# Kernel tuning notes

Measured on AMD Instinct MI355X. Metric: run time of the kernel, lower is better.

Reference implementation:

```python
import jax, jax.numpy as jnp
import numpy as np

D_MODEL = 1024
N_HEADS = 16
D_HEAD = D_MODEL // N_HEADS  # 64
SCALE = 1.0 / float(np.sqrt(D_HEAD))


def setup_inputs() -> dict:
    key = jax.random.key(0)
    kx, kq, kk, kv, ko = jax.random.split(key, 5)
    B, L = 1, 4096
    x = jax.random.normal(kx, (B, L, D_MODEL), dtype=jnp.float32)
    init = 0.02  # small init so softmax isn't saturated
    Wq = jax.random.normal(kq, (D_MODEL, D_MODEL), dtype=jnp.float32) * init
    Wk = jax.random.normal(kk, (D_MODEL, D_MODEL), dtype=jnp.float32) * init
    Wv = jax.random.normal(kv, (D_MODEL, D_MODEL), dtype=jnp.float32) * init
    Wo = jax.random.normal(ko, (D_MODEL, D_MODEL), dtype=jnp.float32) * init
    return {"x": x, "Wq": Wq, "Wk": Wk, "Wv": Wv, "Wo": Wo}


def reference(x, Wq, Wk, Wv, Wo):
    # x: [B, L, d_model]; torch Linear (no bias): y = x @ W.T
    B, L, _ = x.shape

    def split_heads(t):  # [B, L, d_model] -> [B, H, L, Dh]
        return t.reshape(B, L, N_HEADS, D_HEAD).transpose(0, 2, 1, 3)

    q = split_heads(x @ Wq.T)
    k = split_heads(x @ Wk.T)
    v = split_heads(x @ Wv.T)

    # Full (non-flash) attention: explicit [B, H, L, L] scores (causal=False, eval dropout=0)
    scores = jnp.einsum("bhld,bhmd->bhlm", q, k) * SCALE
    attn = jax.nn.softmax(scores, axis=-1)
    out = jnp.einsum("bhlm,bhmd->bhld", attn, v)

    out = out.transpose(0, 2, 1, 3).reshape(B, L, D_MODEL)
    return out @ Wo.T
```

## Files before the change

kernel.cpp:

```cpp
#include <hip/hip_runtime.h>

typedef _Float16 f16_t;
typedef _Float16 f16x4 __attribute__((ext_vector_type(4)));
typedef _Float16 f16x8 __attribute__((ext_vector_type(8)));
typedef float f32x4 __attribute__((ext_vector_type(4)));

#define D_MODEL 1024
#define LSEQ 4096
#define NH 16
#define DH 64
#define QSCALE 0.18033688011112042f

#define GLDS16(g, l)                                                     \
    __builtin_amdgcn_global_load_lds(                                    \
        (const __attribute__((address_space(1))) void*)(g),              \
        (__attribute__((address_space(3))) void*)(l), 16, 0, 0)

#define WAIT_VM0() asm volatile("s_waitcnt vmcnt(0)" ::: "memory")

__global__ __launch_bounds__(256) void cvt_x(const float* __restrict__ in,
                                             f16_t* __restrict__ out, int n) {
    int i = (blockIdx.x * 256 + threadIdx.x) * 4;
    if (i + 3 < n) {
        float4 v = *(const float4*)&in[i];
        alignas(8) f16_t o4[4] = {(f16_t)v.x, (f16_t)v.y, (f16_t)v.z, (f16_t)v.w};
        *(uint2*)&out[i] = *(const uint2*)o4;
    }
}

__global__ __launch_bounds__(256) void cvt_w4(const float* __restrict__ w0,
                                              const float* __restrict__ w1,
                                              const float* __restrict__ w2,
                                              const float* __restrict__ w3,
                                              f16_t* __restrict__ out) {
    const int q = blockIdx.y;
    const float* src = (q == 0) ? w0 : (q == 1) ? w1 : (q == 2) ? w2 : w3;
    const float scale = (q == 0) ? QSCALE : 1.f;
    int i = (blockIdx.x * 256 + threadIdx.x) * 4;
    float4 v = *(const float4*)&src[i];
    alignas(8) f16_t o4[4] = {(f16_t)(v.x * scale), (f16_t)(v.y * scale),
                              (f16_t)(v.z * scale), (f16_t)(v.w * scale)};
    *(uint2*)&out[(size_t)q * (D_MODEL * D_MODEL) + i] = *(const uint2*)o4;
}

__global__ __launch_bounds__(256, 2) void gemm_f16(const f16_t* __restrict__ A,
                                                   const f16_t* __restrict__ B,
                                                   void* __restrict__ Cout,
                                                   int M, int N, int K, int mode) {
    __shared__ f16_t As[2][128 * 32];
    __shared__ f16_t Bs[2][128 * 32];

    const int tid  = threadIdx.x;
    const int wave = tid >> 6;
    const int lane = tid & 63;
    const int quad = lane >> 4;
    const int l16  = lane & 15;
    const int wm = (wave & 1) * 64;
    const int wn = (wave >> 1) * 64;
    const int bm = blockIdx.x * 128;
    const int bn = blockIdx.y * 128;

    f32x4 acc[4][4] = {};
    const int nk = K / 32;

    auto stage = [&](int kt, int b) {
        const int c0 = wave * 2;
        GLDS16(&A[(size_t)(bm + c0 * 16 + l16) * K + kt * 32 + quad * 8],
               &As[b][c0 * 512]);
        GLDS16(&A[(size_t)(bm + (c0 + 1) * 16 + l16) * K + kt * 32 + quad * 8],
               &As[b][(c0 + 1) * 512]);
        GLDS16(&B[(size_t)(bn + c0 * 16 + l16) * K + kt * 32 + quad * 8],
               &Bs[b][c0 * 512]);
        GLDS16(&B[(size_t)(bn + (c0 + 1) * 16 + l16) * K + kt * 32 + quad * 8],
               &Bs[b][(c0 + 1) * 512]);
    };

    stage(0, 0);
    for (int kt = 0; kt < nk; ++kt) {
        const int cb = kt & 1;
        WAIT_VM0();
        __syncthreads();
        if (kt + 1 < nk) stage(kt + 1, cb ^ 1);

        f16x8 af[4], bfr[4];
#pragma unroll
        for (int mt = 0; mt < 4; ++mt)
            af[mt] = *(const f16x8*)&As[cb][((wm >> 4) + mt) * 512 + lane * 8];
#pragma unroll
        for (int nt = 0; nt < 4; ++nt)
            bfr[nt] = *(const f16x8*)&Bs[cb][((wn >> 4) + nt) * 512 + lane * 8];
#pragma unroll
        for (int mt = 0; mt < 4; ++mt)
#pragma unroll
            for (int nt = 0; nt < 4; ++nt)
                acc[mt][nt] = __builtin_amdgcn_mfma_f32_16x16x32_f16(
                    af[mt], bfr[nt], acc[mt][nt], 0, 0, 0);
    }

#pragma unroll
    for (int mt = 0; mt < 4; ++mt)
#pragma unroll
        for (int nt = 0; nt < 4; ++nt)
#pragma unroll
            for (int r = 0; r < 4; ++r) {
                int row = bm + wm + mt * 16 + quad * 4 + r;
                int col = bn + wn + nt * 16 + l16;
                float v = acc[mt][nt][r];
                if (mode == 0) {
                    ((f16_t*)Cout)[((size_t)(col >> 6) * M + row) * 64 + (col & 63)] =
                        (f16_t)v;
                } else {
                    ((float*)Cout)[(size_t)row * N + col] = v;
                }
            }
}

__global__ __launch_bounds__(256) void transpose_v(const f16_t* __restrict__ vh,
                                                   f16_t* __restrict__ vt) {
    __shared__ f16_t Ts[64][72];
    const int t = threadIdx.x;
    const int lt = blockIdx.x;
    const int head = blockIdx.y;

#pragma unroll
    for (int i = 0; i < 2; ++i) {
        int idx = t + i * 256;
        int row = idx >> 3, part = idx & 7;
        *(uint4*)&Ts[row][part * 8] =
            *(const uint4*)&vh[((size_t)head * LSEQ + lt * 64 + row) * DH + part * 8];
    }
    __syncthreads();
#pragma unroll
    for (int i = 0; i < 2; ++i) {
        int idx = t + i * 256;
        int d = idx >> 3, part = idx & 7;
        alignas(16) f16_t p8[8];
#pragma unroll
        for (int j = 0; j < 8; ++j) p8[j] = Ts[part * 8 + j][d];
        *(uint4*)&vt[((size_t)head * DH + d) * LSEQ + lt * 64 + part * 8] =
            *(const uint4*)p8;
    }
}

__global__ __launch_bounds__(256, 2) void attn_kernel(const f16_t* __restrict__ qh,
                                                      const f16_t* __restrict__ kh,
                                                      const f16_t* __restrict__ vt,
                                                      f16_t* __restrict__ ao) {
    __shared__ f16_t Ks[2][8 * 512];
    __shared__ f16_t Vs[2][8 * 512];
    __shared__ f16_t Ps[4][32][72];

    const int tid  = threadIdx.x;
    const int wave = tid >> 6;
    const int lane = tid & 63;
    const int quad = lane >> 4;
    const int l16  = lane & 15;

    const int id = blockIdx.x;
    const int head = (id & 7) * 2 + ((id >> 3) & 1);
    const int qrow0 = (id >> 4) * 128 + wave * 32;

    const f16_t* Q  = qh + (size_t)head * LSEQ * DH;
    const f16_t* K  = kh + (size_t)head * LSEQ * DH;
    const f16_t* Vt = vt + (size_t)head * DH * LSEQ;

    f16x8 qf[2][2];
#pragma unroll
    for (int qt = 0; qt < 2; ++qt)
#pragma unroll
        for (int kc = 0; kc < 2; ++kc)
            qf[qt][kc] = *(const f16x8*)
                &Q[(size_t)(qrow0 + qt * 16 + l16) * DH + kc * 32 + quad * 8];

    f32x4 o[4][2] = {};
    float lp[2] = {0.f, 0.f};

    auto stage = [&](int kt, int b) {
        const int j0 = wave * 2;
#pragma unroll
        for (int jj = 0; jj < 2; ++jj) {
            const int j = j0 + jj, mt = j >> 1, kc = j & 1;
            GLDS16(&K[(size_t)(kt * 64 + mt * 16 + l16) * DH + kc * 32 + quad * 8],
                   &Ks[b][j * 512]);
            GLDS16(&Vt[(size_t)(mt * 16 + l16) * LSEQ + kt * 64 + kc * 32 + quad * 8],
                   &Vs[b][j * 512]);
        }
    };

    const int NT = LSEQ / 64;
    stage(0, 0);
    for (int kt = 0; kt < NT; ++kt) {
        const int cb = kt & 1;
        WAIT_VM0();
        __syncthreads();
        if (kt + 1 < NT) stage(kt + 1, cb ^ 1);

        f16x8 kf[4][2], vf[4][2];
#pragma unroll
        for (int mt = 0; mt < 4; ++mt)
#pragma unroll
            for (int kc = 0; kc < 2; ++kc)
                kf[mt][kc] = *(const f16x8*)&Ks[cb][(mt * 2 + kc) * 512 + lane * 8];
#pragma unroll
        for (int dt = 0; dt < 4; ++dt)
#pragma unroll
            for (int kc = 0; kc < 2; ++kc)
                vf[dt][kc] = *(const f16x8*)&Vs[cb][(dt * 2 + kc) * 512 + lane * 8];

        f32x4 s[4][2] = {};
#pragma unroll
        for (int mt = 0; mt < 4; ++mt)
#pragma unroll
            for (int qt = 0; qt < 2; ++qt)
#pragma unroll
                for (int kc = 0; kc < 2; ++kc)
                    s[mt][qt] = __builtin_amdgcn_mfma_f32_16x16x32_f16(
                        kf[mt][kc], qf[qt][kc], s[mt][qt], 0, 0, 0);

#pragma unroll
        for (int mt = 0; mt < 4; ++mt)
#pragma unroll
            for (int qt = 0; qt < 2; ++qt) {
                float e0 = __builtin_amdgcn_exp2f(s[mt][qt][0]);
                float e1 = __builtin_amdgcn_exp2f(s[mt][qt][1]);
                float e2 = __builtin_amdgcn_exp2f(s[mt][qt][2]);
                float e3 = __builtin_amdgcn_exp2f(s[mt][qt][3]);
                lp[qt] += (e0 + e1) + (e2 + e3);
                f16x4 p = {(f16_t)e0, (f16_t)e1, (f16_t)e2, (f16_t)e3};
                *(f16x4*)&Ps[wave][qt * 16 + l16][mt * 16 + quad * 4] = p;
            }
        __builtin_amdgcn_wave_barrier();

        f16x8 pf[2][2];
#pragma unroll
        for (int qt = 0; qt < 2; ++qt)
#pragma unroll
            for (int kc = 0; kc < 2; ++kc)
                pf[qt][kc] = *(const f16x8*)
                    &Ps[wave][qt * 16 + l16][kc * 32 + quad * 8];

#pragma unroll
        for (int dt = 0; dt < 4; ++dt)
#pragma unroll
            for (int qt = 0; qt < 2; ++qt)
#pragma unroll
                for (int kc = 0; kc < 2; ++kc)
                    o[dt][qt] = __builtin_amdgcn_mfma_f32_16x16x32_f16(
                        vf[dt][kc], pf[qt][kc], o[dt][qt], 0, 0, 0);
        __builtin_amdgcn_wave_barrier();
    }

#pragma unroll
    for (int qt = 0; qt < 2; ++qt) {
        float t = lp[qt];
        t += __shfl_xor(t, 16, 64);
        t += __shfl_xor(t, 32, 64);
        lp[qt] = 1.f / t;
    }
#pragma unroll
    for (int dt = 0; dt < 4; ++dt)
#pragma unroll
        for (int qt = 0; qt < 2; ++qt) {
            f16x4 ov = {(f16_t)(o[dt][qt][0] * lp[qt]),
                        (f16_t)(o[dt][qt][1] * lp[qt]),
                        (f16_t)(o[dt][qt][2] * lp[qt]),
                        (f16_t)(o[dt][qt][3] * lp[qt])};
            int qrow = qrow0 + qt * 16 + l16;
            *(f16x4*)&ao[(size_t)qrow * D_MODEL + head * 64 + dt * 16 + quad * 4] = ov;
        }
}

extern "C" void kernel_launch(void* const* d_in, const int* in_sizes, int n_in,
                              void* d_out, int out_size, void* d_ws, size_t ws_size,
                              hipStream_t stream) {
    const float* x  = (const float*)d_in[0];
    const float* Wq = (const float*)d_in[1];
    const float* Wk = (const float*)d_in[2];
    const float* Wv = (const float*)d_in[3];
    const float* Wo = (const float*)d_in[4];

    f16_t* xb = (f16_t*)d_ws;
    f16_t* wq = xb + (size_t)LSEQ * D_MODEL;
    f16_t* wo = wq + (size_t)3 * D_MODEL * D_MODEL;
    f16_t* qh = wo + (size_t)D_MODEL * D_MODEL;
    f16_t* kh = qh + (size_t)LSEQ * D_MODEL;
    f16_t* vh = kh + (size_t)LSEQ * D_MODEL;
    f16_t* vt = vh + (size_t)LSEQ * D_MODEL;
    f16_t* ao = vt + (size_t)LSEQ * D_MODEL;

    const int nx = LSEQ * D_MODEL;
    cvt_x<<<nx / 1024, 256, 0, stream>>>(x, xb, nx);
    cvt_w4<<<dim3(D_MODEL * D_MODEL / 1024, 4), 256, 0, stream>>>(Wq, Wk, Wv, Wo, wq);

    gemm_f16<<<dim3(LSEQ / 128, 3 * D_MODEL / 128), 256, 0, stream>>>(
        xb, wq, qh, LSEQ, 3 * D_MODEL, D_MODEL, 0);

    transpose_v<<<dim3(LSEQ / 64, NH), 256, 0, stream>>>(vh, vt);

    attn_kernel<<<dim3((LSEQ / 128) * NH), 256, 0, stream>>>(qh, kh, vt, ao);

    gemm_f16<<<dim3(LSEQ / 128, D_MODEL / 128), 256, 0, stream>>>(
        ao, wo, d_out, LSEQ, D_MODEL, D_MODEL, 1);
}
```

Baseline: 273.2 us.

## Triple-buffer GEMM and attention loads and double attention query tile per wave

Both the projection GEMM and the attention kernel move from double to triple buffering of their LDS tiles. They wait with a partial vmcnt so one future stage stays in flight while the current tile is consumed. The attention kernel also gives each wave 64 query rows instead of 32, so every K/V tile loaded into LDS is reused over twice as many queries. That halves the grid to 256 blocks at one block per CU, which cuts latency hiding and raises register pressure. The GEMM's launch bound is raised to 3 blocks per CU to match its larger shared-memory footprint.

```diff
diff --git a/kernel.cpp b/kernel.cpp
--- a/kernel.cpp
+++ b/kernel.cpp
@@ -16,7 +16,7 @@
         (const __attribute__((address_space(1))) void*)(g),              \
         (__attribute__((address_space(3))) void*)(l), 16, 0, 0)
 
-#define WAIT_VM0() asm volatile("s_waitcnt vmcnt(0)" ::: "memory")
+#define WAIT_VM(n) asm volatile("s_waitcnt vmcnt(" #n ")" ::: "memory")
 
 __global__ __launch_bounds__(256) void cvt_x(const float* __restrict__ in,
                                              f16_t* __restrict__ out, int n) {
@@ -43,12 +43,12 @@
     *(uint2*)&out[(size_t)q * (D_MODEL * D_MODEL) + i] = *(const uint2*)o4;
 }
 
-__global__ __launch_bounds__(256, 2) void gemm_f16(const f16_t* __restrict__ A,
+__global__ __launch_bounds__(256, 3) void gemm_f16(const f16_t* __restrict__ A,
                                                    const f16_t* __restrict__ B,
                                                    void* __restrict__ Cout,
                                                    int M, int N, int K, int mode) {
-    __shared__ f16_t As[2][128 * 32];
-    __shared__ f16_t Bs[2][128 * 32];
+    __shared__ alignas(16) f16_t As[3][128 * 32];
+    __shared__ alignas(16) f16_t Bs[3][128 * 32];
 
     const int tid  = threadIdx.x;
     const int wave = tid >> 6;
@@ -76,11 +76,13 @@
     };
 
     stage(0, 0);
+    stage(1, 1);
     for (int kt = 0; kt < nk; ++kt) {
-        const int cb = kt & 1;
-        WAIT_VM0();
+        const int cb = kt % 3;
+        if (kt < nk - 1) WAIT_VM(4);
+        else             WAIT_VM(0);
         __syncthreads();
-        if (kt + 1 < nk) stage(kt + 1, cb ^ 1);
+        if (kt + 2 < nk) stage(kt + 2, (kt + 2) % 3);
 
         f16x8 af[4], bfr[4];
 #pragma unroll
@@ -142,13 +144,13 @@
     }
 }
 
-__global__ __launch_bounds__(256, 2) void attn_kernel(const f16_t* __restrict__ qh,
+__global__ __launch_bounds__(256, 1) void attn_kernel(const f16_t* __restrict__ qh,
                                                       const f16_t* __restrict__ kh,
                                                       const f16_t* __restrict__ vt,
                                                       f16_t* __restrict__ ao) {
-    __shared__ f16_t Ks[2][8 * 512];
-    __shared__ f16_t Vs[2][8 * 512];
-    __shared__ f16_t Ps[4][32][72];
+    __shared__ alignas(16) f16_t Ks[3][8 * 512];
+    __shared__ alignas(16) f16_t Vs[3][8 * 512];
+    __shared__ alignas(16) f16_t Ps[4][64][72];
 
     const int tid  = threadIdx.x;
     const int wave = tid >> 6;
@@ -158,22 +160,22 @@
 
     const int id = blockIdx.x;
     const int head = (id & 7) * 2 + ((id >> 3) & 1);
-    const int qrow0 = (id >> 4) * 128 + wave * 32;
+    const int qrow0 = (id >> 4) * 256 + wave * 64;
 
     const f16_t* Q  = qh + (size_t)head * LSEQ * DH;
     const f16_t* K  = kh + (size_t)head * LSEQ * DH;
     const f16_t* Vt = vt + (size_t)head * DH * LSEQ;
 
-    f16x8 qf[2][2];
-#pragma unroll
-    for (int qt = 0; qt < 2; ++qt)
+    f16x8 qf[4][2];
+#pragma unroll
+    for (int qt = 0; qt < 4; ++qt)
 #pragma unroll
         for (int kc = 0; kc < 2; ++kc)
             qf[qt][kc] = *(const f16x8*)
                 &Q[(size_t)(qrow0 + qt * 16 + l16) * DH + kc * 32 + quad * 8];
 
-    f32x4 o[4][2] = {};
-    float lp[2] = {0.f, 0.f};
+    f32x4 o[4][4] = {};
+    float lp[4] = {0.f, 0.f, 0.f, 0.f};
 
     auto stage = [&](int kt, int b) {
         const int j0 = wave * 2;
@@ -189,11 +191,13 @@
 
     const int NT = LSEQ / 64;
     stage(0, 0);
+    stage(1, 1);
     for (int kt = 0; kt < NT; ++kt) {
-        const int cb = kt & 1;
-        WAIT_VM0();
+        const int cb = kt % 3;
+        if (kt < NT - 1) WAIT_VM(4);
+        else             WAIT_VM(0);
         __syncthreads();
-        if (kt + 1 < NT) stage(kt + 1, cb ^ 1);
+        if (kt + 2 < NT) stage(kt + 2, (kt + 2) % 3);
 
         f16x8 kf[4][2], vf[4][2];
 #pragma unroll
@@ -207,11 +211,11 @@
             for (int kc = 0; kc < 2; ++kc)
                 vf[dt][kc] = *(const f16x8*)&Vs[cb][(dt * 2 + kc) * 512 + lane * 8];
 
-        f32x4 s[4][2] = {};
-#pragma unroll
-        for (int mt = 0; mt < 4; ++mt)
-#pragma unroll
-            for (int qt = 0; qt < 2; ++qt)
+        f32x4 s[4][4] = {};
+#pragma unroll
+        for (int mt = 0; mt < 4; ++mt)
+#pragma unroll
+            for (int qt = 0; qt < 4; ++qt)
 #pragma unroll
                 for (int kc = 0; kc < 2; ++kc)
                     s[mt][qt] = __builtin_amdgcn_mfma_f32_16x16x32_f16(
@@ -220,7 +224,7 @@
 #pragma unroll
         for (int mt = 0; mt < 4; ++mt)
 #pragma unroll
-            for (int qt = 0; qt < 2; ++qt) {
+            for (int qt = 0; qt < 4; ++qt) {
                 float e0 = __builtin_amdgcn_exp2f(s[mt][qt][0]);
                 float e1 = __builtin_amdgcn_exp2f(s[mt][qt][1]);
                 float e2 = __builtin_amdgcn_exp2f(s[mt][qt][2]);
@@ -231,9 +235,9 @@
             }
         __builtin_amdgcn_wave_barrier();
 
-        f16x8 pf[2][2];
-#pragma unroll
-        for (int qt = 0; qt < 2; ++qt)
+        f16x8 pf[4][2];
+#pragma unroll
+        for (int qt = 0; qt < 4; ++qt)
 #pragma unroll
             for (int kc = 0; kc < 2; ++kc)
                 pf[qt][kc] = *(const f16x8*)
@@ -242,7 +246,7 @@
 #pragma unroll
         for (int dt = 0; dt < 4; ++dt)
 #pragma unroll
-            for (int qt = 0; qt < 2; ++qt)
+            for (int qt = 0; qt < 4; ++qt)
 #pragma unroll
                 for (int kc = 0; kc < 2; ++kc)
                     o[dt][qt] = __builtin_amdgcn_mfma_f32_16x16x32_f16(
@@ -251,7 +255,7 @@
     }
 
 #pragma unroll
-    for (int qt = 0; qt < 2; ++qt) {
+    for (int qt = 0; qt < 4; ++qt) {
         float t = lp[qt];
         t += __shfl_xor(t, 16, 64);
         t += __shfl_xor(t, 32, 64);
@@ -260,7 +264,7 @@
 #pragma unroll
     for (int dt = 0; dt < 4; ++dt)
 #pragma unroll
-        for (int qt = 0; qt < 2; ++qt) {
+        for (int qt = 0; qt < 4; ++qt) {
             f16x4 ov = {(f16_t)(o[dt][qt][0] * lp[qt]),
                         (f16_t)(o[dt][qt][1] * lp[qt]),
                         (f16_t)(o[dt][qt][2] * lp[qt]),
@@ -297,7 +301,7 @@
 
     transpose_v<<<dim3(LSEQ / 64, NH), 256, 0, stream>>>(vh, vt);
 
-    attn_kernel<<<dim3((LSEQ / 128) * NH), 256, 0, stream>>>(qh, kh, vt, ao);
+    attn_kernel<<<dim3((LSEQ / 256) * NH), 256, 0, stream>>>(qh, kh, vt, ao);
 
     gemm_f16<<<dim3(LSEQ / 128, D_MODEL / 128), 256, 0, stream>>>(
         ao, wo, d_out, LSEQ, D_MODEL, D_MODEL, 1);
```

After: 304.2 us. 1.11x slower.
